# Kernel optimization log

Measured on AMD Instinct MI355X. Metric: run time of the kernel, lower is better.

Reference implementation:

```python
import jax, jax.numpy as jnp
import numpy as np

B, NPG, F, DEG = 512, 512, 255, 32   # graphs, nodes-per-graph, feat dim, avg degree
N = B * NPG
E = N * DEG
RATIO = 0.5
K = int(np.ceil(RATIO * NPG))        # nodes kept per graph (static)


def setup_inputs() -> dict:
    key = jax.random.key(0)
    k1, k2, k3, k4, k5 = jax.random.split(key, 5)
    out = jax.random.normal(k1, (N, F), jnp.float32)
    z = jax.random.randint(k2, (N,), 0, 101)  # z == 100 marks virtual nodes
    # random edges strictly within each graph (block-contiguous node ids)
    local = jax.random.randint(k3, (2, B, NPG * DEG), 0, NPG)
    offs = (jnp.arange(B) * NPG)[None, :, None]
    edge_index = (local + offs).reshape(2, E)
    batch = jnp.repeat(jnp.arange(B), NPG)
    W = jax.random.normal(k4, (F + 1, 1), jnp.float32) * (1.0 / np.sqrt(F + 1))
    b = jnp.zeros((1,), jnp.float32)
    edge_attr = jax.random.normal(k5, (E, 1), jnp.float32)  # carried but unused by SAGPool scoring
    return dict(out=out, z=z, edge_index=edge_index, batch=batch, W=W, b=b,
                edge_attr=edge_attr)


def gcn_score(x, edge_index, W, b):
    """GCNConv(F+1 -> 1) with self-loops and symmetric normalization."""
    n = x.shape[0]
    h = (x @ W)[:, 0]  # [N] since out_channels == 1
    row, col = edge_index[0], edge_index[1]
    loop = jnp.arange(n)
    row = jnp.concatenate([row, loop])
    col = jnp.concatenate([col, loop])
    deg = jax.ops.segment_sum(jnp.ones_like(col, x.dtype), col, num_segments=n)
    dinv = jnp.where(deg > 0, jax.lax.rsqrt(deg), 0.0)
    norm = dinv[row] * dinv[col]  # deg^-1/2 * deg^-1/2 per edge
    agg = jax.ops.segment_sum(norm * h[row], col, num_segments=n)
    return agg + b[0]


def reference(out, z, edge_index, batch, W, b, edge_attr):
    # concat real/virtual bit
    real = (z != 100).astype(out.dtype)[:, None]
    x = jnp.concatenate([out, real], axis=-1)          # [N, F+1]
    # SAGPooling: score nodes, tanh nonlinearity
    score = jnp.tanh(gcn_score(x, edge_index, W, b))   # [N]
    # per-graph top-k (uniform graph size -> static-shape top_k)
    sv, si = jax.lax.top_k(score.reshape(B, NPG), K)   # [B, K]
    perm = (si + (jnp.arange(B) * NPG)[:, None]).reshape(-1)  # global node ids
    xp = x[perm] * sv.reshape(-1)[:, None]             # gated selected nodes [B*K, F+1]
    # global_mean_pool over pooled batch (k nodes per graph)
    return xp.reshape(B, K, F + 1).mean(axis=1)        # [B, F+1]
```

## Files before the change

kernel.cpp:

```cpp
#include <hip/hip_runtime.h>
#include <math.h>

#define NPG     512
#define B_GR    512
#define FDIM    255
#define DEG     32
#define EPG     (NPG * DEG)
#define N_NODES (B_GR * NPG)
#define E_TOT   (N_NODES * DEG)
#define K_KEEP  256

#define CH_NODES 16
#define CH_FLOATS (CH_NODES * FDIM)
#define CH_F4     (CH_FLOATS / 4)
#define NCHUNK    (NPG / CH_NODES)

__device__ __forceinline__ void lds_dma16(const void* g, void* l) {
    __builtin_amdgcn_global_load_lds(
        (const __attribute__((address_space(1))) unsigned int*)g,
        (__attribute__((address_space(3))) unsigned int*)l, 16, 0, 0);
}

__global__ __launch_bounds__(1024) void k_fused(const float* __restrict__ feat,
                                                const int*   __restrict__ z,
                                                const int*   __restrict__ ei,
                                                const float* __restrict__ W,
                                                const float* __restrict__ bias,
                                                float*       __restrict__ outp) {
    __shared__ __align__(16) float stage[2][CH_FLOATS];
    __shared__ __align__(16) float Wl[256];
    __shared__ __align__(16) float score[NPG];
    __shared__ float h_l[NPG];
    __shared__ float dinv_l[NPG];
    __shared__ float agg[NPG];
    __shared__ float realb[NPG];
    __shared__ int   deg[NPG];
    __shared__ int   rank2[2][NPG];
    __shared__ int   selidx[K_KEEP];
    __shared__ float selsc[K_KEEP];
    __shared__ float red[3][256];
    __shared__ int   cnt;

    const int g     = blockIdx.x;
    const int tid   = threadIdx.x;
    const int nbase = g * NPG;
    const int lane  = tid & 63;
    const int wave  = tid >> 6;

    if (tid < 256) Wl[tid] = W[tid];
    if (tid < NPG) {
        realb[tid] = (z[nbase + tid] != 100) ? 1.f : 0.f;
        deg[tid]   = 1;
        agg[tid]   = 0.f;
    }
    if (tid == 0) cnt = 0;
    __syncthreads();

    {
        const float w0   = Wl[lane];
        const float w64  = Wl[lane + 64];
        const float w128 = Wl[lane + 128];
        const float w192 = (lane < 63) ? Wl[lane + 192] : 0.f;
        const float w255 = Wl[FDIM];
        const char* srcb = (const char*)(feat + (size_t)nbase * FDIM);

        if (tid < CH_F4)
            lds_dma16(srcb + (size_t)tid * 16, (char*)stage[0] + (size_t)tid * 16);
        asm volatile("s_waitcnt vmcnt(0)" ::: "memory");
        __builtin_amdgcn_s_barrier();
        __builtin_amdgcn_sched_barrier(0);

        for (int ch = 0; ch < NCHUNK; ++ch) {
            const float* cur = stage[ch & 1];
            float*       nxt = (float*)stage[(ch & 1) ^ 1];
            if (ch + 1 < NCHUNK && tid < CH_F4)
                lds_dma16(srcb + (size_t)(ch + 1) * 16320 + (size_t)tid * 16,
                          (char*)nxt + (size_t)tid * 16);

            const float* row = cur + wave * FDIM;
            const float  rb  = realb[ch * CH_NODES + wave];
            float acc = (lane == 0) ? rb * w255 : 0.f;
            acc = fmaf(row[lane],       w0,   acc);
            acc = fmaf(row[lane + 64],  w64,  acc);
            acc = fmaf(row[lane + 128], w128, acc);
            if (lane < 63)
                acc = fmaf(row[lane + 192], w192, acc);
#pragma unroll
            for (int off = 32; off; off >>= 1)
                acc += __shfl_down(acc, off, 64);
            if (lane == 0) h_l[ch * CH_NODES + wave] = acc;

            asm volatile("s_waitcnt vmcnt(0)" ::: "memory");
            __builtin_amdgcn_s_barrier();
            __builtin_amdgcn_sched_barrier(0);
        }
    }

    {
        ushort4*    cc4   = (ushort4*)stage;
        const int4* colp4 = (const int4*)(ei + (size_t)E_TOT + (size_t)g * EPG);
        const int4* rowp4 = (const int4*)(ei + (size_t)g * EPG);

#pragma unroll
        for (int it = 0; it < 4; ++it) {
            const int  idx = it * 1024 + tid;
            const int4 c4  = colp4[idx];
            ushort4 u;
            u.x = (unsigned short)(c4.x - nbase);
            u.y = (unsigned short)(c4.y - nbase);
            u.z = (unsigned short)(c4.z - nbase);
            u.w = (unsigned short)(c4.w - nbase);
            cc4[idx] = u;
            atomicAdd(&deg[u.x], 1);
            atomicAdd(&deg[u.y], 1);
            atomicAdd(&deg[u.z], 1);
            atomicAdd(&deg[u.w], 1);
        }
        __syncthreads();

        if (tid < NPG)
            dinv_l[tid] = (float)(1.0 / sqrt((double)deg[tid]));
        __syncthreads();

#pragma unroll
        for (int it = 0; it < 4; ++it) {
            const int     idx = it * 1024 + tid;
            const int4    r4  = rowp4[idx];
            const ushort4 u   = cc4[idx];
            int r;
            r = r4.x - nbase; atomicAdd(&agg[u.x], dinv_l[r] * dinv_l[u.x] * h_l[r]);
            r = r4.y - nbase; atomicAdd(&agg[u.y], dinv_l[r] * dinv_l[u.y] * h_l[r]);
            r = r4.z - nbase; atomicAdd(&agg[u.z], dinv_l[r] * dinv_l[u.z] * h_l[r]);
            r = r4.w - nbase; atomicAdd(&agg[u.w], dinv_l[r] * dinv_l[u.w] * h_l[r]);
        }
        __syncthreads();
    }

    if (tid < NPG)
        score[tid] = tanhf(agg[tid] + dinv_l[tid] * dinv_l[tid] * h_l[tid] + bias[0]);
    __syncthreads();

    {
        const int    node = tid & (NPG - 1);
        const int    half = tid >> 9;
        const float  sc   = score[node];
        const float4* s4p = (const float4*)&score[half * 256];
        int part = 0;
#pragma unroll 8
        for (int i = 0; i < 64; ++i) {
            const float4 s4 = s4p[i];
            const int    j  = half * 256 + i * 4;
            part += (s4.x > sc) || (s4.x == sc && (j + 0) < node);
            part += (s4.y > sc) || (s4.y == sc && (j + 1) < node);
            part += (s4.z > sc) || (s4.z == sc && (j + 2) < node);
            part += (s4.w > sc) || (s4.w == sc && (j + 3) < node);
        }
        rank2[half][node] = part;
    }
    __syncthreads();

    if (tid < NPG) {
        const int rank = rank2[0][tid] + rank2[1][tid];
        if (rank < K_KEEP) {
            const int slot = atomicAdd(&cnt, 1);
            selidx[slot] = tid;
            selsc[slot]  = score[tid];
        }
    }
    __syncthreads();

    {
        const int f = tid & 255;
        const int q = tid >> 8;
        float acc = 0.f;
        if (f < FDIM) {
            const float* fb = feat + (size_t)nbase * FDIM + f;
#pragma unroll 8
            for (int s = q; s < K_KEEP; s += 4)
                acc = fmaf(selsc[s], fb[(size_t)selidx[s] * FDIM], acc);
        } else {
#pragma unroll 8
            for (int s = q; s < K_KEEP; s += 4)
                acc = fmaf(selsc[s], realb[selidx[s]], acc);
        }
        if (q) red[q - 1][f] = acc;
        __syncthreads();
        if (q == 0)
            outp[(size_t)g * 256 + f] =
                (acc + red[0][f] + red[1][f] + red[2][f]) * (1.f / K_KEEP);
    }
}

extern "C" void kernel_launch(void* const* d_in, const int* in_sizes, int n_in,
                              void* d_out, int out_size, void* d_ws, size_t ws_size,
                              hipStream_t stream) {
    const float* feat = (const float*)d_in[0];
    const int*   z    = (const int*)  d_in[1];
    const int*   ei   = (const int*)  d_in[2];
    const float* W    = (const float*)d_in[4];
    const float* bias = (const float*)d_in[5];
    float* outp = (float*)d_out;

    k_fused<<<B_GR, 1024, 0, stream>>>(feat, z, ei, W, bias, outp);
}
```

Measured before the change: 118.4 us.

## Overlap degree counting with feature streaming and simplify GCN aggregation

Degree atomics on the column indices now run inside the feature-projection chunk loop, every 8th chunk, so the edge-index loads overlap the LDS DMA streaming. The aggregation is refactored algebraically: h is pre-scaled by dinv, agg is seeded with the self-loop term, and the final score uses a single multiply by dinv. Because of this, the ushort column cache in LDS is dropped and columns are reloaded from global memory. The gather in the final pooling is batched eight loads at a time for more memory-level parallelism, and launch bounds gain a min-blocks hint. The trade-off is an extra global read of the column indices and some added register pressure.

```diff
diff --git a/kernel.cpp b/kernel.cpp
--- a/kernel.cpp
+++ b/kernel.cpp
@@ -21,12 +21,12 @@
         (__attribute__((address_space(3))) unsigned int*)l, 16, 0, 0);
 }
 
-__global__ __launch_bounds__(1024) void k_fused(const float* __restrict__ feat,
-                                                const int*   __restrict__ z,
-                                                const int*   __restrict__ ei,
-                                                const float* __restrict__ W,
-                                                const float* __restrict__ bias,
-                                                float*       __restrict__ outp) {
+__global__ __launch_bounds__(1024, 8) void k_fused(const float* __restrict__ feat,
+                                                   const int*   __restrict__ z,
+                                                   const int*   __restrict__ ei,
+                                                   const float* __restrict__ W,
+                                                   const float* __restrict__ bias,
+                                                   float*       __restrict__ outp) {
     __shared__ __align__(16) float stage[2][CH_FLOATS];
     __shared__ __align__(16) float Wl[256];
     __shared__ __align__(16) float score[NPG];
@@ -47,11 +47,13 @@
     const int lane  = tid & 63;
     const int wave  = tid >> 6;
 
+    const int4* colp4 = (const int4*)(ei + (size_t)E_TOT + (size_t)g * EPG);
+    const int4* rowp4 = (const int4*)(ei + (size_t)g * EPG);
+
     if (tid < 256) Wl[tid] = W[tid];
     if (tid < NPG) {
         realb[tid] = (z[nbase + tid] != 100) ? 1.f : 0.f;
         deg[tid]   = 1;
-        agg[tid]   = 0.f;
     }
     if (tid == 0) cnt = 0;
     __syncthreads();
@@ -73,13 +75,18 @@
         for (int ch = 0; ch < NCHUNK; ++ch) {
             const float* cur = stage[ch & 1];
             float*       nxt = (float*)stage[(ch & 1) ^ 1];
+
+            int4 c4;
+            const bool do_deg = ((ch & 7) == 0);
+            if (do_deg)
+                c4 = colp4[(ch >> 3) * 1024 + tid];
+
             if (ch + 1 < NCHUNK && tid < CH_F4)
                 lds_dma16(srcb + (size_t)(ch + 1) * 16320 + (size_t)tid * 16,
                           (char*)nxt + (size_t)tid * 16);
 
             const float* row = cur + wave * FDIM;
-            const float  rb  = realb[ch * CH_NODES + wave];
-            float acc = (lane == 0) ? rb * w255 : 0.f;
+            float acc = (lane == 0) ? realb[ch * CH_NODES + wave] * w255 : 0.f;
             acc = fmaf(row[lane],       w0,   acc);
             acc = fmaf(row[lane + 64],  w64,  acc);
             acc = fmaf(row[lane + 128], w128, acc);
@@ -90,54 +97,43 @@
                 acc += __shfl_down(acc, off, 64);
             if (lane == 0) h_l[ch * CH_NODES + wave] = acc;
 
+            if (do_deg) {
+                atomicAdd(&deg[c4.x - nbase], 1);
+                atomicAdd(&deg[c4.y - nbase], 1);
+                atomicAdd(&deg[c4.z - nbase], 1);
+                atomicAdd(&deg[c4.w - nbase], 1);
+            }
+
             asm volatile("s_waitcnt vmcnt(0)" ::: "memory");
             __builtin_amdgcn_s_barrier();
             __builtin_amdgcn_sched_barrier(0);
         }
     }
-
-    {
-        ushort4*    cc4   = (ushort4*)stage;
-        const int4* colp4 = (const int4*)(ei + (size_t)E_TOT + (size_t)g * EPG);
-        const int4* rowp4 = (const int4*)(ei + (size_t)g * EPG);
-
-#pragma unroll
-        for (int it = 0; it < 4; ++it) {
-            const int  idx = it * 1024 + tid;
-            const int4 c4  = colp4[idx];
-            ushort4 u;
-            u.x = (unsigned short)(c4.x - nbase);
-            u.y = (unsigned short)(c4.y - nbase);
-            u.z = (unsigned short)(c4.z - nbase);
-            u.w = (unsigned short)(c4.w - nbase);
-            cc4[idx] = u;
-            atomicAdd(&deg[u.x], 1);
-            atomicAdd(&deg[u.y], 1);
-            atomicAdd(&deg[u.z], 1);
-            atomicAdd(&deg[u.w], 1);
-        }
-        __syncthreads();
-
-        if (tid < NPG)
-            dinv_l[tid] = (float)(1.0 / sqrt((double)deg[tid]));
-        __syncthreads();
-
-#pragma unroll
-        for (int it = 0; it < 4; ++it) {
-            const int     idx = it * 1024 + tid;
-            const int4    r4  = rowp4[idx];
-            const ushort4 u   = cc4[idx];
-            int r;
-            r = r4.x - nbase; atomicAdd(&agg[u.x], dinv_l[r] * dinv_l[u.x] * h_l[r]);
-            r = r4.y - nbase; atomicAdd(&agg[u.y], dinv_l[r] * dinv_l[u.y] * h_l[r]);
-            r = r4.z - nbase; atomicAdd(&agg[u.z], dinv_l[r] * dinv_l[u.z] * h_l[r]);
-            r = r4.w - nbase; atomicAdd(&agg[u.w], dinv_l[r] * dinv_l[u.w] * h_l[r]);
-        }
-        __syncthreads();
-    }
+    __syncthreads();
+
+    if (tid < NPG) {
+        const float di = (float)(1.0 / sqrt((double)deg[tid]));
+        dinv_l[tid] = di;
+        const float v = di * h_l[tid];
+        h_l[tid] = v;
+        agg[tid] = v;
+    }
+    __syncthreads();
+
+#pragma unroll
+    for (int it = 0; it < 4; ++it) {
+        const int  idx = it * 1024 + tid;
+        const int4 r4  = rowp4[idx];
+        const int4 c4  = colp4[idx];
+        atomicAdd(&agg[c4.x - nbase], h_l[r4.x - nbase]);
+        atomicAdd(&agg[c4.y - nbase], h_l[r4.y - nbase]);
+        atomicAdd(&agg[c4.z - nbase], h_l[r4.z - nbase]);
+        atomicAdd(&agg[c4.w - nbase], h_l[r4.w - nbase]);
+    }
+    __syncthreads();
 
     if (tid < NPG)
-        score[tid] = tanhf(agg[tid] + dinv_l[tid] * dinv_l[tid] * h_l[tid] + bias[0]);
+        score[tid] = tanhf(fmaf(agg[tid], dinv_l[tid], bias[0]));
     __syncthreads();
 
     {
@@ -175,11 +171,22 @@
         float acc = 0.f;
         if (f < FDIM) {
             const float* fb = feat + (size_t)nbase * FDIM + f;
-#pragma unroll 8
-            for (int s = q; s < K_KEEP; s += 4)
-                acc = fmaf(selsc[s], fb[(size_t)selidx[s] * FDIM], acc);
+#pragma unroll
+            for (int k = 0; k < 64; k += 8) {
+                int   is[8]; float ss[8]; float tv[8];
+#pragma unroll
+                for (int j = 0; j < 8; ++j) {
+                    is[j] = selidx[q + 4 * (k + j)];
+                    ss[j] = selsc [q + 4 * (k + j)];
+                }
+#pragma unroll
+                for (int j = 0; j < 8; ++j)
+                    tv[j] = fb[(size_t)is[j] * FDIM];
+#pragma unroll
+                for (int j = 0; j < 8; ++j)
+                    acc = fmaf(ss[j], tv[j], acc);
+            }
         } else {
-#pragma unroll 8
             for (int s = q; s < K_KEEP; s += 4)
                 acc = fmaf(selsc[s], realb[selidx[s]], acc);
         }
```

After: 124.5 us. 5.1% more time.

## Prescale GCN messages by dinv, prefetch edges, row-wise gather for pooled mean

Applied to the files above, without the earlier changes.

Folds the source-side deg^-1/2 into a per-node value and seeds agg with the self-loop term, so each edge atomic adds one LDS value and the destination-side scale is applied once per node. Edge row/col indices are now loaded into registers up front, and __syncthreads is replaced by a lighter lgkmcnt wait plus s_barrier. The final gated mean pool has each wave read whole contiguous selected rows and reduce into an LDS accumulator with atomics, instead of column-strided reads. This trades extra register pressure and LDS atomic contention for fewer per-edge loads and more coalesced feature reads.

```diff
diff --git a/kernel.cpp b/kernel.cpp
--- a/kernel.cpp
+++ b/kernel.cpp
@@ -21,16 +21,18 @@
         (__attribute__((address_space(3))) unsigned int*)l, 16, 0, 0);
 }
 
+#define BAR_LGKM() asm volatile("s_waitcnt lgkmcnt(0)\n\ts_barrier" ::: "memory")
+
 __global__ __launch_bounds__(1024) void k_fused(const float* __restrict__ feat,
                                                 const int*   __restrict__ z,
                                                 const int*   __restrict__ ei,
                                                 const float* __restrict__ W,
                                                 const float* __restrict__ bias,
                                                 float*       __restrict__ outp) {
-    __shared__ __align__(16) float stage[2][CH_FLOATS];
+    __shared__ __align__(16) char stagebuf[32768];
     __shared__ __align__(16) float Wl[256];
     __shared__ __align__(16) float score[NPG];
-    __shared__ float h_l[NPG];
+    __shared__ float v_l[NPG];
     __shared__ float dinv_l[NPG];
     __shared__ float agg[NPG];
     __shared__ float realb[NPG];
@@ -38,7 +40,6 @@
     __shared__ int   rank2[2][NPG];
     __shared__ int   selidx[K_KEEP];
     __shared__ float selsc[K_KEEP];
-    __shared__ float red[3][256];
     __shared__ int   cnt;
 
     const int g     = blockIdx.x;
@@ -47,16 +48,19 @@
     const int lane  = tid & 63;
     const int wave  = tid >> 6;
 
+    const int4* colp4 = (const int4*)(ei + (size_t)E_TOT + (size_t)g * EPG);
+    const int4* rowp4 = (const int4*)(ei + (size_t)g * EPG);
+
     if (tid < 256) Wl[tid] = W[tid];
     if (tid < NPG) {
         realb[tid] = (z[nbase + tid] != 100) ? 1.f : 0.f;
         deg[tid]   = 1;
-        agg[tid]   = 0.f;
     }
     if (tid == 0) cnt = 0;
     __syncthreads();
 
     {
+        float (*stage)[CH_FLOATS] = (float (*)[CH_FLOATS])stagebuf;
         const float w0   = Wl[lane];
         const float w64  = Wl[lane + 64];
         const float w128 = Wl[lane + 128];
@@ -72,14 +76,13 @@
 
         for (int ch = 0; ch < NCHUNK; ++ch) {
             const float* cur = stage[ch & 1];
-            float*       nxt = (float*)stage[(ch & 1) ^ 1];
+            float*       nxt = stage[(ch & 1) ^ 1];
             if (ch + 1 < NCHUNK && tid < CH_F4)
                 lds_dma16(srcb + (size_t)(ch + 1) * 16320 + (size_t)tid * 16,
                           (char*)nxt + (size_t)tid * 16);
 
             const float* row = cur + wave * FDIM;
-            const float  rb  = realb[ch * CH_NODES + wave];
-            float acc = (lane == 0) ? rb * w255 : 0.f;
+            float acc = (lane == 0) ? realb[ch * CH_NODES + wave] * w255 : 0.f;
             acc = fmaf(row[lane],       w0,   acc);
             acc = fmaf(row[lane + 64],  w64,  acc);
             acc = fmaf(row[lane + 128], w128, acc);
@@ -88,63 +91,70 @@
 #pragma unroll
             for (int off = 32; off; off >>= 1)
                 acc += __shfl_down(acc, off, 64);
-            if (lane == 0) h_l[ch * CH_NODES + wave] = acc;
+            if (lane == 0) v_l[ch * CH_NODES + wave] = acc;
 
             asm volatile("s_waitcnt vmcnt(0)" ::: "memory");
             __builtin_amdgcn_s_barrier();
             __builtin_amdgcn_sched_barrier(0);
         }
     }
-
-    {
-        ushort4*    cc4   = (ushort4*)stage;
-        const int4* colp4 = (const int4*)(ei + (size_t)E_TOT + (size_t)g * EPG);
-        const int4* rowp4 = (const int4*)(ei + (size_t)g * EPG);
+    BAR_LGKM();
+
+    {
+        ushort4* cc4 = (ushort4*)stagebuf;
+
+        int4 c4v[4], r4v[4];
+#pragma unroll
+        for (int it = 0; it < 4; ++it) c4v[it] = colp4[it * 1024 + tid];
+#pragma unroll
+        for (int it = 0; it < 4; ++it) r4v[it] = rowp4[it * 1024 + tid];
 
 #pragma unroll
         for (int it = 0; it < 4; ++it) {
-            const int  idx = it * 1024 + tid;
-            const int4 c4  = colp4[idx];
+            const int4 c4 = c4v[it];
             ushort4 u;
             u.x = (unsigned short)(c4.x - nbase);
             u.y = (unsigned short)(c4.y - nbase);
             u.z = (unsigned short)(c4.z - nbase);
             u.w = (unsigned short)(c4.w - nbase);
-            cc4[idx] = u;
+            cc4[it * 1024 + tid] = u;
             atomicAdd(&deg[u.x], 1);
             atomicAdd(&deg[u.y], 1);
             atomicAdd(&deg[u.z], 1);
             atomicAdd(&deg[u.w], 1);
         }
-        __syncthreads();
-
-        if (tid < NPG)
-            dinv_l[tid] = (float)(1.0 / sqrt((double)deg[tid]));
-        __syncthreads();
+        BAR_LGKM();
+
+        if (tid < NPG) {
+            const float di = (float)(1.0 / sqrt((double)deg[tid]));
+            dinv_l[tid] = di;
+            const float v = di * v_l[tid];
+            v_l[tid] = v;
+            agg[tid] = v;
+        }
+        BAR_LGKM();
 
 #pragma unroll
         for (int it = 0; it < 4; ++it) {
-            const int     idx = it * 1024 + tid;
-            const int4    r4  = rowp4[idx];
-            const ushort4 u   = cc4[idx];
-            int r;
-            r = r4.x - nbase; atomicAdd(&agg[u.x], dinv_l[r] * dinv_l[u.x] * h_l[r]);
-            r = r4.y - nbase; atomicAdd(&agg[u.y], dinv_l[r] * dinv_l[u.y] * h_l[r]);
-            r = r4.z - nbase; atomicAdd(&agg[u.z], dinv_l[r] * dinv_l[u.z] * h_l[r]);
-            r = r4.w - nbase; atomicAdd(&agg[u.w], dinv_l[r] * dinv_l[u.w] * h_l[r]);
-        }
-        __syncthreads();
+            const ushort4 u  = cc4[it * 1024 + tid];
+            const int4    r4 = r4v[it];
+            atomicAdd(&agg[u.x], v_l[r4.x - nbase]);
+            atomicAdd(&agg[u.y], v_l[r4.y - nbase]);
+            atomicAdd(&agg[u.z], v_l[r4.z - nbase]);
+            atomicAdd(&agg[u.w], v_l[r4.w - nbase]);
+        }
+        BAR_LGKM();
     }
 
     if (tid < NPG)
-        score[tid] = tanhf(agg[tid] + dinv_l[tid] * dinv_l[tid] * h_l[tid] + bias[0]);
-    __syncthreads();
-
-    {
-        const int    node = tid & (NPG - 1);
-        const int    half = tid >> 9;
-        const float  sc   = score[node];
-        const float4* s4p = (const float4*)&score[half * 256];
+        score[tid] = tanhf(fmaf(agg[tid], dinv_l[tid], bias[0]));
+    BAR_LGKM();
+
+    {
+        const int     node = tid & (NPG - 1);
+        const int     half = tid >> 9;
+        const float   sc   = score[node];
+        const float4* s4p  = (const float4*)&score[half * 256];
         int part = 0;
 #pragma unroll 8
         for (int i = 0; i < 64; ++i) {
@@ -157,7 +167,7 @@
         }
         rank2[half][node] = part;
     }
-    __syncthreads();
+    BAR_LGKM();
 
     if (tid < NPG) {
         const int rank = rank2[0][tid] + rank2[1][tid];
@@ -167,27 +177,38 @@
             selsc[slot]  = score[tid];
         }
     }
-    __syncthreads();
-
-    {
-        const int f = tid & 255;
-        const int q = tid >> 8;
-        float acc = 0.f;
-        if (f < FDIM) {
-            const float* fb = feat + (size_t)nbase * FDIM + f;
-#pragma unroll 8
-            for (int s = q; s < K_KEEP; s += 4)
-                acc = fmaf(selsc[s], fb[(size_t)selidx[s] * FDIM], acc);
-        } else {
-#pragma unroll 8
-            for (int s = q; s < K_KEEP; s += 4)
-                acc = fmaf(selsc[s], realb[selidx[s]], acc);
-        }
-        if (q) red[q - 1][f] = acc;
-        __syncthreads();
-        if (q == 0)
-            outp[(size_t)g * 256 + f] =
-                (acc + red[0][f] + red[1][f] + red[2][f]) * (1.f / K_KEEP);
+    BAR_LGKM();
+
+    {
+        float* outacc = (float*)rank2;
+        if (tid < 256) outacc[tid] = 0.f;
+        BAR_LGKM();
+
+        const float* base = feat + (size_t)nbase * FDIM;
+        float a0 = 0.f, a1 = 0.f, a2 = 0.f, a3 = 0.f;
+#pragma unroll 4
+        for (int k = 0; k < 16; ++k) {
+            const int   s   = wave + 16 * k;
+            const int   idx = selidx[s];
+            const float sc  = selsc[s];
+            const float* rp = base + (size_t)idx * FDIM;
+            const float v0 = rp[lane];
+            const float v1 = rp[lane + 64];
+            const float v2 = rp[lane + 128];
+            const float v3 = (lane < 63) ? rp[lane + 192] : realb[idx];
+            a0 = fmaf(sc, v0, a0);
+            a1 = fmaf(sc, v1, a1);
+            a2 = fmaf(sc, v2, a2);
+            a3 = fmaf(sc, v3, a3);
+        }
+        atomicAdd(&outacc[lane],       a0);
+        atomicAdd(&outacc[lane + 64],  a1);
+        atomicAdd(&outacc[lane + 128], a2);
+        atomicAdd(&outacc[lane + 192], a3);
+        BAR_LGKM();
+
+        if (tid < 256)
+            outp[(size_t)g * 256 + tid] = outacc[tid] * (1.f / K_KEEP);
     }
 }
 
```

Result: slower. 175.1 us (+47.8%).
